# Optimization experiments

Measured on AMD Instinct MI355X. Metric: run time of the kernel, lower is better.

Reference implementation:

```python
import jax, jax.numpy as jnp
import numpy as np

B, S, HID = 2, 2048, 2048
H, KVH, D = 16, 8, 128           # query heads, kv heads, head_dim
G = H // KVH                      # num_key_value_groups
EPS = 1e-6
SCALE = D ** -0.5
ROPE_THETA = 1e6


def _rope_tables():
    inv_freq = 1.0 / (ROPE_THETA ** (jnp.arange(0, D, 2, dtype=jnp.float32) / D))
    freqs = jnp.arange(S, dtype=jnp.float32)[:, None] * inv_freq[None, :]   # [S, D/2]
    emb = jnp.concatenate([freqs, freqs], axis=-1)                          # [S, D]
    cos = jnp.broadcast_to(jnp.cos(emb)[None], (B, S, D))
    sin = jnp.broadcast_to(jnp.sin(emb)[None], (B, S, D))
    return cos, sin


def setup_inputs() -> dict:
    key = jax.random.key(0)
    ks = jax.random.split(key, 6)
    hidden_states = jax.random.normal(ks[0], (B, S, HID), jnp.float32)
    cos, sin = _rope_tables()
    w = 0.02
    Wq = jax.random.normal(ks[1], (HID, H * D * 2), jnp.float32) * w  # gated: q + gate
    Wk = jax.random.normal(ks[2], (HID, KVH * D), jnp.float32) * w
    Wv = jax.random.normal(ks[3], (HID, KVH * D), jnp.float32) * w
    Wo = jax.random.normal(ks[4], (H * D, HID), jnp.float32) * w
    q_norm_w = jnp.ones((D,), jnp.float32)
    k_norm_w = jnp.ones((D,), jnp.float32)
    return {"hidden_states": hidden_states, "cos": cos, "sin": sin,
            "Wq": Wq, "Wk": Wk, "Wv": Wv, "Wo": Wo,
            "q_norm_w": q_norm_w, "k_norm_w": k_norm_w}


def _rms_norm(x, w):
    # per-head RMSNorm over last dim (head_dim), computed in fp32
    var = jnp.mean(jnp.square(x.astype(jnp.float32)), axis=-1, keepdims=True)
    return (x * jax.lax.rsqrt(var + EPS)) * w


def _rotate_half(x):
    x1, x2 = x[..., : D // 2], x[..., D // 2:]
    return jnp.concatenate([-x2, x1], axis=-1)


def reference(hidden_states, cos, sin, Wq, Wk, Wv, Wo, q_norm_w, k_norm_w):
    # q_proj with output gate
    mixed_q = hidden_states @ Wq                         # [B,S,H*2D]
    mixed_q = mixed_q.reshape(B, S, H, 2 * D)
    q, gate = mixed_q[..., :D], mixed_q[..., D:]          # [B,S,H,D] each
    gate = gate.reshape(B, S, H * D)
    k = (hidden_states @ Wk).reshape(B, S, KVH, D)
    v = (hidden_states @ Wv).reshape(B, S, KVH, D)

    # per-head QK RMSNorm, then to [B, heads, S, D]
    q = _rms_norm(q, q_norm_w).transpose(0, 2, 1, 3)      # [B,H,S,D]
    k = _rms_norm(k, k_norm_w).transpose(0, 2, 1, 3)      # [B,KVH,S,D]
    v = v.transpose(0, 2, 1, 3)                           # [B,KVH,S,D]

    # RoPE (cos/sin broadcast over head dim)
    c, s = cos[:, None], sin[:, None]                     # [B,1,S,D]
    q = q * c + _rotate_half(q) * s
    k = k * c + _rotate_half(k) * s

    # GQA causal attention without materializing repeated K/V
    qg = q.reshape(B, KVH, G, S, D)
    scores = jnp.einsum('bkgqd,bkld->bkgql', qg, k) * SCALE   # [B,KVH,G,S,S]
    causal = jnp.tril(jnp.ones((S, S), dtype=bool))
    scores = jnp.where(causal, scores, jnp.finfo(scores.dtype).min)
    probs = jax.nn.softmax(scores, axis=-1)
    out = jnp.einsum('bkgql,bkld->bkgqd', probs, v)           # [B,KVH,G,S,D]
    out = out.reshape(B, H, S, D).transpose(0, 2, 1, 3).reshape(B, S, H * D)

    # sigmoid-gated output, then o_proj
    out = out * jax.nn.sigmoid(gate)
    return out @ Wo
```

## Files before the change

kernel.cpp:

```cpp
#include <hip/hip_runtime.h>
#include <hip/hip_bf16.h>

#define B_ 2
#define S_ 2048
#define HID_ 2048
#define H_ 16
#define KVH_ 8
#define D_ 128
#define G_ 2
#define EPS_ 1e-6f
#define SCALE_ 0.08838834764831845f
#define SCALE2_ 0.1275313760443445f
#define NQKV 6144

typedef __hip_bfloat16 bf16;
typedef __attribute__((ext_vector_type(8))) short s8v;
typedef __attribute__((ext_vector_type(4))) float f4v;

__device__ __forceinline__ unsigned short f2b(float f) {
    __hip_bfloat16 h = __float2bfloat16(f);
    return *reinterpret_cast<unsigned short*>(&h);
}
__device__ __forceinline__ float b2f(short u) {
    unsigned int x = ((unsigned int)(unsigned short)u) << 16;
    return __builtin_bit_cast(float, x);
}

__device__ __forceinline__ f4v MFMA(s8v a, s8v b, f4v c) {
    return __builtin_amdgcn_mfma_f32_16x16x32_bf16(a, b, c, 0, 0, 0);
}

__device__ __forceinline__ void gl_lds16(const void* g, void* l) {
    __builtin_amdgcn_global_load_lds(
        (const __attribute__((address_space(1))) void*)g,
        (__attribute__((address_space(3))) void*)l, 16, 0, 0);
}

__device__ __forceinline__ void cstore(float* p, float v) { *p = v; }
__device__ __forceinline__ void cstore(short* p, float v) { *p = (short)f2b(v); }

template <int CTRL>
__device__ __forceinline__ float dpp_f(float x) {
    return __builtin_bit_cast(float,
        __builtin_amdgcn_update_dpp(0, __builtin_bit_cast(int, x), CTRL, 0xF, 0xF, true));
}
__device__ __forceinline__ float red16_max(float v) {
    v = fmaxf(v, dpp_f<0xB1>(v));
    v = fmaxf(v, dpp_f<0x4E>(v));
    v = fmaxf(v, dpp_f<0x124>(v));
    v = fmaxf(v, dpp_f<0x128>(v));
    return v;
}
__device__ __forceinline__ float red16_sum(float v) {
    v += dpp_f<0xB1>(v);
    v += dpp_f<0x4E>(v);
    v += dpp_f<0x124>(v);
    v += dpp_f<0x128>(v);
    return v;
}

__global__ __launch_bounds__(256) void f2bf_kernel(const float* __restrict__ in,
                                                   short* __restrict__ out, int n4) {
    int i = blockIdx.x * 256 + threadIdx.x;
    if (i >= n4) return;
    const float4 v = *(const float4*)(in + (size_t)i * 4);
    ushort4 o;
    o.x = f2b(v.x); o.y = f2b(v.y); o.z = f2b(v.z); o.w = f2b(v.w);
    *(ushort4*)(out + (size_t)i * 4) = o;
}

__global__ __launch_bounds__(256) void transpose_conv(const float* __restrict__ in,
                                                      short* __restrict__ out,
                                                      int K, int N) {
    __shared__ short t[32][33];
    const int n0 = blockIdx.x * 32, k0 = blockIdx.y * 32;
    const int tx = threadIdx.x, ty = threadIdx.y;
#pragma unroll
    for (int j = 0; j < 4; j++) {
        const int r = ty + j * 8;
        t[r][tx] = (short)f2b(in[(size_t)(k0 + r) * N + n0 + tx]);
    }
    __syncthreads();
#pragma unroll
    for (int j = 0; j < 4; j++) {
        const int r = ty + j * 8;
        out[(size_t)(n0 + r) * K + k0 + tx] = t[tx][r];
    }
}

__global__ __launch_bounds__(256) void transpose_v(const short* __restrict__ in,
                                                   short* __restrict__ out) {
    __shared__ short t[32][33];
    const int s0 = blockIdx.x * 32, d0 = blockIdx.y * 32, bk = blockIdx.z;
    const int b = bk / KVH_, kvh = bk % KVH_;
    const short* ip = in + (size_t)b * S_ * NQKV + kvh * D_;
    const int tx = threadIdx.x, ty = threadIdx.y;
#pragma unroll
    for (int j = 0; j < 4; j++) {
        const int r = ty + j * 8;
        t[r][tx] = ip[(size_t)(s0 + r) * NQKV + d0 + tx];
    }
    __syncthreads();
#pragma unroll
    for (int j = 0; j < 4; j++) {
        const int r = ty + j * 8;
        out[((size_t)bk * D_ + d0 + r) * S_ + s0 + tx] = t[tx][r];
    }
}

__global__ __launch_bounds__(512, 2) void gemm256(const short* __restrict__ A,
                                                  const short* __restrict__ Bt,
                                                  short* __restrict__ C,
                                                  int M, int N, int K) {
    __shared__ __align__(16) short As[3][256][32];
    __shared__ __align__(16) short Bs[3][256][32];
    const int tid = threadIdx.x;
    const int w = tid >> 6, l = tid & 63;
    const int lr = l & 15, g = l >> 4;
    const int nwg = gridDim.x * gridDim.y;
    int bid = blockIdx.y * gridDim.x + blockIdx.x;
    bid = (bid & 7) * (nwg >> 3) + (bid >> 3);
    const int bx = bid % gridDim.x, by = bid / gridDim.x;
    const int row0 = by * 256, col0 = bx * 256;
    const int wr = w >> 2, wc = w & 3;

    f4v acc[8][4];
#pragma unroll
    for (int i = 0; i < 8; i++)
#pragma unroll
        for (int j = 0; j < 4; j++) acc[i][j] = (f4v)0.f;

    const int srow = l >> 2;
    const int schunk = (l & 3) ^ ((l >> 3) & 3);
    const int rdslot = (g ^ ((lr >> 1) & 3)) * 8;

    auto stageA = [&](int buf, int t) {
        const int kt = t * 32;
#pragma unroll
        for (int i = 0; i < 2; i++) {
            const int rb = w * 32 + i * 16;
            gl_lds16(A + (size_t)(row0 + rb + srow) * K + kt + schunk * 8,
                     &As[buf][rb][0]);
        }
    };
    auto stageB = [&](int buf, int t) {
        const int kt = t * 32;
#pragma unroll
        for (int i = 0; i < 2; i++) {
            const int rb = w * 32 + i * 16;
            gl_lds16(Bt + (size_t)(col0 + rb + srow) * K + kt + schunk * 8,
                     &Bs[buf][rb][0]);
        }
    };

    const int nt = K >> 5;
    stageA(0, 0); stageB(0, 0);
    stageA(1, 1); stageB(1, 1);

#pragma unroll 1
    for (int t = 0; t < nt; t++) {
        const int buf = t % 3;
        const int nbuf = (t + 2) % 3;

        __builtin_amdgcn_sched_barrier(0);
        if (t + 1 < nt) {
            asm volatile("s_waitcnt vmcnt(4)" ::: "memory");
        } else {
            asm volatile("s_waitcnt vmcnt(0)" ::: "memory");
        }
        __builtin_amdgcn_sched_barrier(0);
        __builtin_amdgcn_s_barrier();
        __builtin_amdgcn_sched_barrier(0);

        s8v b[4], a[4];
#pragma unroll
        for (int ni = 0; ni < 4; ni++)
            b[ni] = *(const s8v*)&Bs[buf][wc * 64 + ni * 16 + lr][rdslot];
#pragma unroll
        for (int mi = 0; mi < 4; mi++)
            a[mi] = *(const s8v*)&As[buf][wr * 128 + mi * 16 + lr][rdslot];
        if (t + 2 < nt) stageA(nbuf, t + 2);
        __builtin_amdgcn_s_setprio(1);
#pragma unroll
        for (int mi = 0; mi < 4; mi++)
#pragma unroll
            for (int ni = 0; ni < 4; ni++)
                acc[mi][ni] = MFMA(a[mi], b[ni], acc[mi][ni]);
        __builtin_amdgcn_s_setprio(0);
        __builtin_amdgcn_s_barrier();
        __builtin_amdgcn_sched_barrier(0);

        s8v a2[4];
#pragma unroll
        for (int mi = 0; mi < 4; mi++)
            a2[mi] = *(const s8v*)&As[buf][wr * 128 + (4 + mi) * 16 + lr][rdslot];
        if (t + 2 < nt) stageB(nbuf, t + 2);
        __builtin_amdgcn_s_setprio(1);
#pragma unroll
        for (int mi = 0; mi < 4; mi++)
#pragma unroll
            for (int ni = 0; ni < 4; ni++)
                acc[4 + mi][ni] = MFMA(a2[mi], b[ni], acc[4 + mi][ni]);
        __builtin_amdgcn_s_setprio(0);
    }

#pragma unroll
    for (int mi = 0; mi < 8; mi++)
#pragma unroll
        for (int ni = 0; ni < 4; ni++) {
            const int row = row0 + wr * 128 + mi * 16 + g * 4;
            const int col = col0 + wc * 64 + ni * 16 + lr;
#pragma unroll
            for (int j = 0; j < 4; j++)
                cstore(&C[(size_t)(row + j) * N + col], acc[mi][ni][j]);
        }
}

template <typename CT, int GATED>
__global__ __launch_bounds__(256) void gemm_bt(const short* __restrict__ A,
                                               const short* __restrict__ Bt,
                                               CT* __restrict__ C,
                                               int M, int N, int K) {
    __shared__ __align__(16) short As[2][128][32];
    __shared__ __align__(16) short Bs[2][128][32];
    const int tid = threadIdx.x;
    const int w = tid >> 6, l = tid & 63;
    const int lr = l & 15, g = l >> 4;
    const int nwg = gridDim.x * gridDim.y;
    int bid = blockIdx.y * gridDim.x + blockIdx.x;
    bid = (bid & 7) * (nwg >> 3) + (bid >> 3);
    const int bx = bid % gridDim.x, by = bid / gridDim.x;
    const int row0 = by * 128, col0 = bx * 128;
    const int wr = w >> 1, wc = w & 1;

    f4v acc[4][4];
#pragma unroll
    for (int i = 0; i < 4; i++)
#pragma unroll
        for (int j = 0; j < 4; j++) acc[i][j] = (f4v)0.f;

    const int srow = l >> 2;
    const int sg = (l & 3) ^ ((srow >> 1) & 3);

    auto stage = [&](int buf, int kt) {
        const int k = kt + sg * 8;
#pragma unroll
        for (int i = 0; i < 2; i++) {
            const int rb = (w * 2 + i) * 16;
            size_t aoff;
            if constexpr (GATED)
                aoff = (size_t)(row0 + rb + srow) * NQKV + ((k >> 7) << 8) + (k & 127);
            else
                aoff = (size_t)(row0 + rb + srow) * K + k;
            gl_lds16(A + aoff, &As[buf][rb][0]);
            gl_lds16(Bt + (size_t)(col0 + rb + srow) * K + k, &Bs[buf][rb][0]);
        }
    };

    const int nt = K >> 5;
    stage(0, 0);
    stage(1, 32);
    const int rdslot = (g ^ ((lr >> 1) & 3)) * 8;

#pragma unroll 1
    for (int t = 0; t < nt; t++) {
        const int cur = t & 1;
        if (t + 1 < nt) {
            asm volatile("s_waitcnt vmcnt(4)" ::: "memory");
        } else {
            asm volatile("s_waitcnt vmcnt(0)" ::: "memory");
        }
        __builtin_amdgcn_s_barrier();
        __builtin_amdgcn_sched_barrier(0);

        s8v a[4], b[4];
#pragma unroll
        for (int mi = 0; mi < 4; mi++)
            a[mi] = *(const s8v*)&As[cur][wr * 64 + mi * 16 + lr][rdslot];
#pragma unroll
        for (int ni = 0; ni < 4; ni++)
            b[ni] = *(const s8v*)&Bs[cur][wc * 64 + ni * 16 + lr][rdslot];

        asm volatile("s_waitcnt lgkmcnt(0)" ::: "memory");
        __builtin_amdgcn_sched_barrier(0);
        __builtin_amdgcn_s_barrier();
        __builtin_amdgcn_sched_barrier(0);

        if (t + 2 < nt) stage(cur, (t + 2) * 32);

#pragma unroll
        for (int mi = 0; mi < 4; mi++)
#pragma unroll
            for (int ni = 0; ni < 4; ni++)
                acc[mi][ni] = MFMA(a[mi], b[ni], acc[mi][ni]);
    }

#pragma unroll
    for (int mi = 0; mi < 4; mi++)
#pragma unroll
        for (int ni = 0; ni < 4; ni++) {
            const int row = row0 + wr * 64 + mi * 16 + g * 4;
            const int col = col0 + wc * 64 + ni * 16 + lr;
#pragma unroll
            for (int j = 0; j < 4; j++)
                cstore(&C[(size_t)(row + j) * N + col], acc[mi][ni][j]);
        }
}

__global__ __launch_bounds__(128) void norm_rope(const bf16* __restrict__ src,
                                                 const float* __restrict__ normw,
                                                 const float* __restrict__ cosb,
                                                 const float* __restrict__ sinb,
                                                 bf16* __restrict__ dst,
                                                 int NH, int rowStride, int chanStride) {
    const int idx = blockIdx.x;
    const int h = idx % NH;
    const int s = (idx / NH) % S_;
    const int b = idx / (NH * S_);
    const int d = threadIdx.x;

    const size_t src_i = (size_t)(b * S_ + s) * rowStride + h * chanStride + d;
    const size_t dst_i = (((size_t)b * NH + h) * S_ + s) * D_ + d;

    float x = __bfloat162float(src[src_i]);
    float sq = x * x;
#pragma unroll
    for (int o = 32; o > 0; o >>= 1) sq += __shfl_down(sq, o);
    __shared__ float red[2];
    __shared__ float sh[128];
    if ((d & 63) == 0) red[d >> 6] = sq;
    __syncthreads();
    const float var = (red[0] + red[1]) * (1.f / 128.f);
    const float xn = x * rsqrtf(var + EPS_) * normw[d];
    sh[d] = xn;
    __syncthreads();
    const float rot = (d < 64) ? -sh[d + 64] : sh[d - 64];
    const size_t cs_i = ((size_t)b * S_ + s) * D_ + d;
    dst[dst_i] = __float2bfloat16(xn * cosb[cs_i] + rot * sinb[cs_i]);
}

__global__ __launch_bounds__(256) void flash_mfma(const short* __restrict__ qro,
                                                  const short* __restrict__ kro,
                                                  const short* __restrict__ vt,
                                                  short* __restrict__ qkv) {
    __shared__ __align__(16) short Ks[2][64][128];
    __shared__ __align__(16) short Vs[2][128][64];
    __shared__ __align__(16) short Pl[4][16][84];

    const int tid = threadIdx.x;
    const int w = tid >> 6, l = tid & 63;
    const int lr = l & 15, g = l >> 4;
    const int bx = blockIdx.x;
    const int bh = blockIdx.y;
    const int b = bh >> 4, h = bh & 15;
    const int kvh = h >> 1;

    const short* qbase = qro + (size_t)(b * H_ + h) * S_ * D_;
    const short* kbase = kro + (size_t)(b * KVH_ + kvh) * S_ * D_;
    const short* vbase = vt + (size_t)(b * KVH_ + kvh) * D_ * S_;

    auto stage = [&](int buf, int kt) {
        const int kb0 = kt * 64;
#pragma unroll
        for (int i = 0; i < 4; i++) {
            const int li = w * 4 + i;
            {
                const int r = li * 4 + (l >> 4);
                const int sgk = (l & 15) ^ (r & 7);
                gl_lds16(kbase + (size_t)(kb0 + r) * D_ + sgk * 8, &Ks[buf][li * 4][0]);
            }
            {
                const int r = li * 8 + (l >> 3);
                const int sgv = (l & 7) ^ (r & 7);
                gl_lds16(vbase + (size_t)r * S_ + kb0 + sgv * 8, &Vs[buf][li * 8][0]);
            }
        }
    };

#pragma unroll 1
    for (int seg = 0; seg < 2; seg++) {
        const int qt = seg ? bx : (31 - bx);
        const int q0 = qt * 64;
        const int qw0 = q0 + w * 16;

        if (seg) __syncthreads();

        s8v qa[4];
#pragma unroll
        for (int kc = 0; kc < 4; kc++)
            qa[kc] = *(const s8v*)(qbase + (size_t)(qw0 + lr) * D_ + kc * 32 + g * 8);

        f4v oacc[8];
#pragma unroll
        for (int i = 0; i < 8; i++) oacc[i] = (f4v)0.f;
        float m[4] = {-3e38f, -3e38f, -3e38f, -3e38f};
        float lsum[4] = {0.f, 0.f, 0.f, 0.f};

        const int nkt = qt + 1;
        stage(0, 0);
        int cur = 0;
        for (int kt = 0; kt < nkt; kt++) {
            __syncthreads();
            if (kt + 1 < nkt) stage(cur ^ 1, kt + 1);
            const int kb0 = kt * 64;

            f4v sacc[4];
#pragma unroll
            for (int ni = 0; ni < 4; ni++) sacc[ni] = (f4v)0.f;
            __builtin_amdgcn_s_setprio(1);
#pragma unroll
            for (int ni = 0; ni < 4; ni++) {
                const int r = ni * 16 + lr;
#pragma unroll
                for (int kc = 0; kc < 4; kc++) {
                    const int ph = (kc * 4 + g) ^ (r & 7);
                    const s8v kb = *(const s8v*)&Ks[cur][r][ph * 8];
                    sacc[ni] = MFMA(qa[kc], kb, sacc[ni]);
                }
            }
            __builtin_amdgcn_s_setprio(0);

            const bool masked = (kt == qt);
            float p[4][4], tmax[4];
#pragma unroll
            for (int j = 0; j < 4; j++) {
                float v0 = -3e38f;
#pragma unroll
                for (int ni = 0; ni < 4; ni++) {
                    float sc = sacc[ni][j] * SCALE2_;
                    if (masked && (kb0 + ni * 16 + lr > qw0 + g * 4 + j)) sc = -3e38f;
                    p[ni][j] = sc;
                    v0 = fmaxf(v0, sc);
                }
                tmax[j] = v0;
            }
#pragma unroll
            for (int j = 0; j < 4; j++) tmax[j] = red16_max(tmax[j]);

            bool needb = false;
#pragma unroll
            for (int j = 0; j < 4; j++) needb = needb || (tmax[j] > m[j] + 7.f);
            const bool doresc = __any((int)needb);

            float cj[4], psum[4];
#pragma unroll
            for (int j = 0; j < 4; j++) {
                float mn = m[j];
                if (doresc) {
                    mn = fmaxf(m[j], tmax[j]);
                    cj[j] = __builtin_amdgcn_exp2f(m[j] - mn);
                    m[j] = mn;
                }
                float ps = 0.f;
#pragma unroll
                for (int ni = 0; ni < 4; ni++) {
                    const float e = __builtin_amdgcn_exp2f(p[ni][j] - mn);
                    p[ni][j] = e;
                    ps += e;
                }
                psum[j] = ps;
            }

#pragma unroll
            for (int ni = 0; ni < 4; ni++)
#pragma unroll
                for (int j = 0; j < 4; j++)
                    Pl[w][g * 4 + j][ni * 16 + lr] = (short)f2b(p[ni][j]);

#pragma unroll
            for (int j = 0; j < 4; j++) psum[j] = red16_sum(psum[j]);

            if (doresc) {
#pragma unroll
                for (int j = 0; j < 4; j++) lsum[j] = lsum[j] * cj[j] + psum[j];
#pragma unroll
                for (int di = 0; di < 8; di++)
#pragma unroll
                    for (int j = 0; j < 4; j++) oacc[di][j] *= cj[j];
            } else {
#pragma unroll
                for (int j = 0; j < 4; j++) lsum[j] += psum[j];
            }

            __builtin_amdgcn_s_setprio(1);
#pragma unroll
            for (int kk = 0; kk < 2; kk++) {
                const s8v pa = *(const s8v*)&Pl[w][lr][kk * 32 + g * 8];
#pragma unroll
                for (int di = 0; di < 8; di++) {
                    const int r = di * 16 + lr;
                    const int ph = (kk * 4 + g) ^ (r & 7);
                    const s8v vb = *(const s8v*)&Vs[cur][r][ph * 8];
                    oacc[di] = MFMA(pa, vb, oacc[di]);
                }
            }
            __builtin_amdgcn_s_setprio(0);
            cur ^= 1;
        }

        float linv[4];
#pragma unroll
        for (int j = 0; j < 4; j++) linv[j] = 1.f / lsum[j];
#pragma unroll
        for (int di = 0; di < 8; di++) {
            const int d = di * 16 + lr;
#pragma unroll
            for (int j = 0; j < 4; j++) {
                const int q = qw0 + g * 4 + j;
                const size_t base = (size_t)(b * S_ + q) * NQKV + h * 256;
                const float gate = b2f(qkv[base + 128 + d]);
                const float o = oacc[di][j] * linv[j] * (1.f / (1.f + __expf(-gate)));
                qkv[base + d] = (short)f2b(o);
            }
        }
    }
}

extern "C" void kernel_launch(void* const* d_in, const int* in_sizes, int n_in,
                              void* d_out, int out_size, void* d_ws, size_t ws_size,
                              hipStream_t stream) {
    const float* hs = (const float*)d_in[0];
    const float* cosb = (const float*)d_in[1];
    const float* sinb = (const float*)d_in[2];
    const float* Wq = (const float*)d_in[3];
    const float* Wk = (const float*)d_in[4];
    const float* Wv = (const float*)d_in[5];
    const float* Wo = (const float*)d_in[6];
    const float* qnw = (const float*)d_in[7];
    const float* knw = (const float*)d_in[8];
    float* out = (float*)d_out;

    short* ws = (short*)d_ws;
    short* Wot = ws;
    short* Wt  = ws + 4194304;
    short* hsb = ws + 16777216;
    short* qkv = ws + 25165824;
    short* qro = Wt;
    short* kro = Wt + 8388608;
    short* vtb = hsb;

    const int M = B_ * S_;
    const dim3 t32x8(32, 8, 1);

    f2bf_kernel<<<8192, 256, 0, stream>>>(hs, hsb, 2097152);
    transpose_conv<<<dim3(128, 64), t32x8, 0, stream>>>(Wq, Wt, HID_, 4096);
    transpose_conv<<<dim3(32, 64), t32x8, 0, stream>>>(Wk, Wt + (size_t)4096 * 2048, HID_, 1024);
    transpose_conv<<<dim3(32, 64), t32x8, 0, stream>>>(Wv, Wt + (size_t)5120 * 2048, HID_, 1024);
    transpose_conv<<<dim3(64, 64), t32x8, 0, stream>>>(Wo, Wot, 2048, 2048);

    gemm256<<<dim3(24, 16), 512, 0, stream>>>(hsb, Wt, qkv, M, NQKV, HID_);

    norm_rope<<<dim3(B_ * S_ * H_), 128, 0, stream>>>((const bf16*)qkv, qnw, cosb, sinb,
                                                      (bf16*)qro, H_, NQKV, 256);
    norm_rope<<<dim3(B_ * S_ * KVH_), 128, 0, stream>>>((const bf16*)(qkv + 4096), knw, cosb, sinb,
                                                        (bf16*)kro, KVH_, NQKV, 128);

    transpose_v<<<dim3(64, 4, 16), t32x8, 0, stream>>>(qkv + 5120, vtb);

    flash_mfma<<<dim3(16, 32), 256, 0, stream>>>(qro, kro, vtb, qkv);

    gemm_bt<float, 1><<<dim3(16, 32), 256, 0, stream>>>(qkv, Wot, out, M, HID_, 2048);
}
```

Measured before the change: 326.0 us.

## Double flash-attention query tile to 128 rows per block

Each wave now handles 32 query rows (two 16-row MFMA tiles) instead of 16, so each block covers 128 queries and reuses every staged K/V tile for twice as many rows. This halves the K/V global-to-LDS traffic and the barrier count per unit of work. The grid shrinks to 8x32 blocks and register use roughly doubles (launch bounds set to one block per CU). That risks lower occupancy, fewer blocks to fill the CUs, and coarser causal load balance.

New measurement: 361.2 us. +10.8%, slower.

```diff
diff --git a/kernel.cpp b/kernel.cpp
--- a/kernel.cpp
+++ b/kernel.cpp
@@ -339,13 +339,13 @@
     dst[dst_i] = __float2bfloat16(xn * cosb[cs_i] + rot * sinb[cs_i]);
 }
 
-__global__ __launch_bounds__(256) void flash_mfma(const short* __restrict__ qro,
-                                                  const short* __restrict__ kro,
-                                                  const short* __restrict__ vt,
-                                                  short* __restrict__ qkv) {
+__global__ __launch_bounds__(256, 1) void flash_mfma(const short* __restrict__ qro,
+                                                     const short* __restrict__ kro,
+                                                     const short* __restrict__ vt,
+                                                     short* __restrict__ qkv) {
     __shared__ __align__(16) short Ks[2][64][128];
     __shared__ __align__(16) short Vs[2][128][64];
-    __shared__ __align__(16) short Pl[4][16][84];
+    __shared__ __align__(16) short Pl[4][32][84];
 
     const int tid = threadIdx.x;
     const int w = tid >> 6, l = tid & 63;
@@ -379,24 +379,32 @@
 
 #pragma unroll 1
     for (int seg = 0; seg < 2; seg++) {
-        const int qt = seg ? bx : (31 - bx);
-        const int q0 = qt * 64;
-        const int qw0 = q0 + w * 16;
+        const int qt = seg ? bx : (15 - bx);
+        const int q0 = qt * 128;
+        const int qw0 = q0 + w * 32;
 
         if (seg) __syncthreads();
 
-        s8v qa[4];
-#pragma unroll
-        for (int kc = 0; kc < 4; kc++)
-            qa[kc] = *(const s8v*)(qbase + (size_t)(qw0 + lr) * D_ + kc * 32 + g * 8);
-
-        f4v oacc[8];
-#pragma unroll
-        for (int i = 0; i < 8; i++) oacc[i] = (f4v)0.f;
-        float m[4] = {-3e38f, -3e38f, -3e38f, -3e38f};
-        float lsum[4] = {0.f, 0.f, 0.f, 0.f};
-
-        const int nkt = qt + 1;
+        s8v qa[2][4];
+#pragma unroll
+        for (int mi = 0; mi < 2; mi++)
+#pragma unroll
+            for (int kc = 0; kc < 4; kc++)
+                qa[mi][kc] = *(const s8v*)(qbase + (size_t)(qw0 + mi * 16 + lr) * D_ +
+                                           kc * 32 + g * 8);
+
+        f4v oacc[2][8];
+#pragma unroll
+        for (int mi = 0; mi < 2; mi++)
+#pragma unroll
+            for (int i = 0; i < 8; i++) oacc[mi][i] = (f4v)0.f;
+        float m[2][4], lsum[2][4];
+#pragma unroll
+        for (int mi = 0; mi < 2; mi++)
+#pragma unroll
+            for (int j = 0; j < 4; j++) { m[mi][j] = -3e38f; lsum[mi][j] = 0.f; }
+
+        const int nkt = 2 * (qt + 1);
         stage(0, 0);
         int cur = 0;
         for (int kt = 0; kt < nkt; kt++) {
@@ -404,9 +412,11 @@
             if (kt + 1 < nkt) stage(cur ^ 1, kt + 1);
             const int kb0 = kt * 64;
 
-            f4v sacc[4];
-#pragma unroll
-            for (int ni = 0; ni < 4; ni++) sacc[ni] = (f4v)0.f;
+            f4v sacc[2][4];
+#pragma unroll
+            for (int mi = 0; mi < 2; mi++)
+#pragma unroll
+                for (int ni = 0; ni < 4; ni++) sacc[mi][ni] = (f4v)0.f;
             __builtin_amdgcn_s_setprio(1);
 #pragma unroll
             for (int ni = 0; ni < 4; ni++) {
@@ -415,104 +425,133 @@
                 for (int kc = 0; kc < 4; kc++) {
                     const int ph = (kc * 4 + g) ^ (r & 7);
                     const s8v kb = *(const s8v*)&Ks[cur][r][ph * 8];
-                    sacc[ni] = MFMA(qa[kc], kb, sacc[ni]);
+                    sacc[0][ni] = MFMA(qa[0][kc], kb, sacc[0][ni]);
+                    sacc[1][ni] = MFMA(qa[1][kc], kb, sacc[1][ni]);
                 }
             }
             __builtin_amdgcn_s_setprio(0);
 
-            const bool masked = (kt == qt);
-            float p[4][4], tmax[4];
-#pragma unroll
-            for (int j = 0; j < 4; j++) {
-                float v0 = -3e38f;
-#pragma unroll
-                for (int ni = 0; ni < 4; ni++) {
-                    float sc = sacc[ni][j] * SCALE2_;
-                    if (masked && (kb0 + ni * 16 + lr > qw0 + g * 4 + j)) sc = -3e38f;
-                    p[ni][j] = sc;
-                    v0 = fmaxf(v0, sc);
+            const bool masked = (kt >= nkt - 2);
+            float p[2][4][4], tmax[2][4];
+#pragma unroll
+            for (int mi = 0; mi < 2; mi++)
+#pragma unroll
+                for (int j = 0; j < 4; j++) {
+                    float v0 = -3e38f;
+#pragma unroll
+                    for (int ni = 0; ni < 4; ni++) {
+                        float sc = sacc[mi][ni][j] * SCALE2_;
+                        if (masked && (kb0 + ni * 16 + lr > qw0 + mi * 16 + g * 4 + j))
+                            sc = -3e38f;
+                        p[mi][ni][j] = sc;
+                        v0 = fmaxf(v0, sc);
+                    }
+                    tmax[mi][j] = v0;
                 }
-                tmax[j] = v0;
+#pragma unroll
+            for (int mi = 0; mi < 2; mi++)
+#pragma unroll
+                for (int j = 0; j < 4; j++) tmax[mi][j] = red16_max(tmax[mi][j]);
+
+            bool needb = false;
+#pragma unroll
+            for (int mi = 0; mi < 2; mi++)
+#pragma unroll
+                for (int j = 0; j < 4; j++)
+                    needb = needb || (tmax[mi][j] > m[mi][j] + 7.f);
+            const bool doresc = __any((int)needb);
+
+            float cj[2][4], psum[2][4];
+#pragma unroll
+            for (int mi = 0; mi < 2; mi++)
+#pragma unroll
+                for (int j = 0; j < 4; j++) {
+                    float mn = m[mi][j];
+                    if (doresc) {
+                        mn = fmaxf(m[mi][j], tmax[mi][j]);
+                        cj[mi][j] = __builtin_amdgcn_exp2f(m[mi][j] - mn);
+                        m[mi][j] = mn;
+                    }
+                    float ps = 0.f;
+#pragma unroll
+                    for (int ni = 0; ni < 4; ni++) {
+                        const float e = __builtin_amdgcn_exp2f(p[mi][ni][j] - mn);
+                        p[mi][ni][j] = e;
+                        ps += e;
+                    }
+                    psum[mi][j] = ps;
+                }
+
+#pragma unroll
+            for (int mi = 0; mi < 2; mi++)
+#pragma unroll
+                for (int ni = 0; ni < 4; ni++)
+#pragma unroll
+                    for (int j = 0; j < 4; j++)
+                        Pl[w][mi * 16 + g * 4 + j][ni * 16 + lr] =
+                            (short)f2b(p[mi][ni][j]);
+
+#pragma unroll
+            for (int mi = 0; mi < 2; mi++)
+#pragma unroll
+                for (int j = 0; j < 4; j++) psum[mi][j] = red16_sum(psum[mi][j]);
+
+            if (doresc) {
+#pragma unroll
+                for (int mi = 0; mi < 2; mi++) {
+#pragma unroll
+                    for (int j = 0; j < 4; j++)
+                        lsum[mi][j] = lsum[mi][j] * cj[mi][j] + psum[mi][j];
+#pragma unroll
+                    for (int di = 0; di < 8; di++)
+#pragma unroll
+                        for (int j = 0; j < 4; j++) oacc[mi][di][j] *= cj[mi][j];
+                }
+            } else {
+#pragma unroll
+                for (int mi = 0; mi < 2; mi++)
+#pragma unroll
+                    for (int j = 0; j < 4; j++) lsum[mi][j] += psum[mi][j];
             }
-#pragma unroll
-            for (int j = 0; j < 4; j++) tmax[j] = red16_max(tmax[j]);
-
-            bool needb = false;
-#pragma unroll
-            for (int j = 0; j < 4; j++) needb = needb || (tmax[j] > m[j] + 7.f);
-            const bool doresc = __any((int)needb);
-
-            float cj[4], psum[4];
-#pragma unroll
-            for (int j = 0; j < 4; j++) {
-                float mn = m[j];
-                if (doresc) {
-                    mn = fmaxf(m[j], tmax[j]);
-                    cj[j] = __builtin_amdgcn_exp2f(m[j] - mn);
-                    m[j] = mn;
-                }
-                float ps = 0.f;
-#pragma unroll
-                for (int ni = 0; ni < 4; ni++) {
-                    const float e = __builtin_amdgcn_exp2f(p[ni][j] - mn);
-                    p[ni][j] = e;
-                    ps += e;
-                }
-                psum[j] = ps;
-            }
-
-#pragma unroll
-            for (int ni = 0; ni < 4; ni++)
-#pragma unroll
-                for (int j = 0; j < 4; j++)
-                    Pl[w][g * 4 + j][ni * 16 + lr] = (short)f2b(p[ni][j]);
-
-#pragma unroll
-            for (int j = 0; j < 4; j++) psum[j] = red16_sum(psum[j]);
-
-            if (doresc) {
-#pragma unroll
-                for (int j = 0; j < 4; j++) lsum[j] = lsum[j] * cj[j] + psum[j];
-#pragma unroll
-                for (int di = 0; di < 8; di++)
-#pragma unroll
-                    for (int j = 0; j < 4; j++) oacc[di][j] *= cj[j];
-            } else {
-#pragma unroll
-                for (int j = 0; j < 4; j++) lsum[j] += psum[j];
-            }
 
             __builtin_amdgcn_s_setprio(1);
 #pragma unroll
             for (int kk = 0; kk < 2; kk++) {
-                const s8v pa = *(const s8v*)&Pl[w][lr][kk * 32 + g * 8];
+                const s8v pa0 = *(const s8v*)&Pl[w][lr][kk * 32 + g * 8];
+                const s8v pa1 = *(const s8v*)&Pl[w][16 + lr][kk * 32 + g * 8];
 #pragma unroll
                 for (int di = 0; di < 8; di++) {
                     const int r = di * 16 + lr;
                     const int ph = (kk * 4 + g) ^ (r & 7);
                     const s8v vb = *(const s8v*)&Vs[cur][r][ph * 8];
-                    oacc[di] = MFMA(pa, vb, oacc[di]);
+                    oacc[0][di] = MFMA(pa0, vb, oacc[0][di]);
+                    oacc[1][di] = MFMA(pa1, vb, oacc[1][di]);
                 }
             }
             __builtin_amdgcn_s_setprio(0);
             cur ^= 1;
         }
 
-        float linv[4];
-#pragma unroll
-        for (int j = 0; j < 4; j++) linv[j] = 1.f / lsum[j];
-#pragma unroll
-        for (int di = 0; di < 8; di++) {
-            const int d = di * 16 + lr;
-#pragma unroll
-            for (int j = 0; j < 4; j++) {
-                const int q = qw0 + g * 4 + j;
-                const size_t base = (size_t)(b * S_ + q) * NQKV + h * 256;
-                const float gate = b2f(qkv[base + 128 + d]);
-                const float o = oacc[di][j] * linv[j] * (1.f / (1.f + __expf(-gate)));
-                qkv[base + d] = (short)f2b(o);
+        float linv[2][4];
+#pragma unroll
+        for (int mi = 0; mi < 2; mi++)
+#pragma unroll
+            for (int j = 0; j < 4; j++) linv[mi][j] = 1.f / lsum[mi][j];
+#pragma unroll
+        for (int mi = 0; mi < 2; mi++)
+#pragma unroll
+            for (int di = 0; di < 8; di++) {
+                const int d = di * 16 + lr;
+#pragma unroll
+                for (int j = 0; j < 4; j++) {
+                    const int q = qw0 + mi * 16 + g * 4 + j;
+                    const size_t base = (size_t)(b * S_ + q) * NQKV + h * 256;
+                    const float gate = b2f(qkv[base + 128 + d]);
+                    const float o = oacc[mi][di][j] * linv[mi][j] *
+                                    (1.f / (1.f + __expf(-gate)));
+                    qkv[base + d] = (short)f2b(o);
+                }
             }
-        }
     }
 }
 
@@ -557,7 +596,7 @@
 
     transpose_v<<<dim3(64, 4, 16), t32x8, 0, stream>>>(qkv + 5120, vtb);
 
-    flash_mfma<<<dim3(16, 32), 256, 0, stream>>>(qro, kro, vtb, qkv);
+    flash_mfma<<<dim3(8, 32), 256, 0, stream>>>(qro, kro, vtb, qkv);
 
     gemm_bt<float, 1><<<dim3(16, 32), 256, 0, stream>>>(qkv, Wot, out, M, HID_, 2048);
 }
```
